# Kernel tuning notes

Measured on AMD Instinct MI355X. Metric: run time of the kernel, lower is better.

Reference implementation:

```python
import jax, jax.numpy as jnp
import numpy as np
from functools import partial

B, F, H, G, S = 8192, 16, 128, 4, 20  # batch, features, hidden, goals, SUBSTEPS
A_IZH, B_IZH, C_IZH, D_IZH = 0.02, 0.2, -65.0, 8.0  # Izhikevich 'RS' params
RATE_DECAY = 0.9
GAMMA, LR = 0.95, 1e-3


def izh_step(v, u, rate, I):
    """One Izhikevich substep (dt=1): returns new (v, u, rate, spike)."""
    v_new = v + (0.04 * v * v + 5.0 * v + 140.0 - u + I)
    u_new = u + A_IZH * (B_IZH * v - u)
    spike = (v_new >= 30.0).astype(v.dtype)
    v_new = jnp.where(spike > 0, C_IZH, v_new)
    u_new = u_new + spike * D_IZH
    rate_new = RATE_DECAY * rate + (1.0 - RATE_DECAY) * spike
    return v_new, u_new, rate_new, spike


def build_features(energy, threat, food_visible, goal, cls_probs, DA_, NA_):
    # [B,16] = [4 scalars | one-hot goal (4) | cls_probs (5) | DA | NA | hunger]
    base = jnp.stack([energy / 100.0, threat, food_visible, 1.0 - energy / 100.0], axis=-1)
    onehot = jax.nn.one_hot(goal, G, dtype=base.dtype)
    tail = jnp.stack([DA_, NA_, jnp.maximum(0.0, 0.5 - energy / 100.0)], axis=-1)
    return jnp.concatenate([base, onehot, cls_probs, tail], axis=-1)


def setup_inputs() -> dict:
    key = jax.random.key(0)
    ks = jax.random.split(key, 16)
    energy = jax.random.uniform(ks[0], (B,)) * 100.0
    threat = jax.random.uniform(ks[1], (B,))
    food_visible = jax.random.uniform(ks[2], (B,))
    goal = jax.random.randint(ks[3], (B,), 0, G)
    prev_goal = jax.random.randint(ks[4], (B,), 0, G)
    DA_ = jax.random.uniform(ks[5], (B,))
    NA_ = jax.random.uniform(ks[6], (B,))
    reward = jax.random.normal(ks[7], (B,)) * 0.5
    cls_probs = jax.nn.softmax(jax.random.normal(ks[8], (B, 5)), axis=-1)
    a_in = 0.5 * np.sqrt(6.0 / (F + H))   # xavier_uniform gain 0.5
    a_out = 0.3 * np.sqrt(6.0 / (H + G))  # xavier_uniform gain 0.3
    W_in_w = jax.random.uniform(ks[9], (B, H, F), minval=-a_in, maxval=a_in)
    W_in_b = jax.random.uniform(ks[10], (B, H), minval=-1.0, maxval=1.0) / np.sqrt(F)
    W_out_w = jax.random.uniform(ks[11], (B, G, H), minval=-a_out, maxval=a_out)
    W_out_b = jax.random.uniform(ks[12], (B, G), minval=-1.0, maxval=1.0) / np.sqrt(H)
    hv = jnp.full((B, H), -65.0)
    hu = B_IZH * hv
    hrate = jnp.zeros((B, H))
    vv = jnp.full((B, G), -65.0)
    vu = B_IZH * vv
    vrate = jnp.zeros((B, G))
    elig_in = jnp.zeros((B, H, F))
    elig_out = jnp.zeros((B, G, H))
    prev_values = jnp.zeros((B, G))
    prev_features = jax.random.uniform(ks[13], (B, F))
    noise = jax.random.normal(ks[14], (S, B, H))
    return dict(energy=energy, threat=threat, food_visible=food_visible, goal=goal,
                prev_goal=prev_goal, DA_=DA_, NA_=NA_, reward=reward, cls_probs=cls_probs,
                W_in_w=W_in_w, W_in_b=W_in_b, W_out_w=W_out_w, W_out_b=W_out_b,
                hv=hv, hu=hu, hrate=hrate, vv=vv, vu=vu, vrate=vrate,
                elig_in=elig_in, elig_out=elig_out, prev_values=prev_values,
                prev_features=prev_features, noise=noise)


def reference(energy, threat, food_visible, goal, prev_goal, DA_, NA_, reward, cls_probs,
              W_in_w, W_in_b, W_out_w, W_out_b, hv, hu, hrate, vv, vu, vrate,
              elig_in, elig_out, prev_values, prev_features, noise):
    features = build_features(energy, threat, food_visible, goal, cls_probs, DA_, NA_)  # [B,F]
    I_in = jnp.einsum('bhf,bf->bh', W_in_w, features) + W_in_b
    I_in = I_in * (5.0 / (jnp.mean(jnp.abs(I_in), axis=-1, keepdims=True) + 1e-8))

    def step(carry, nz):
        hv, hu, hrate, vv, vu, vrate, hsp, vsp = carry
        hv, hu, hrate, sp_h = izh_step(hv, hu, hrate, I_in + 0.3 * nz)
        I_out = jnp.einsum('bgh,bh->bg', W_out_w, hrate) + W_out_b
        I_out = I_out * (4.0 / (jnp.mean(jnp.abs(I_out), axis=-1, keepdims=True) + 1e-8))
        vv, vu, vrate, sp_v = izh_step(vv, vu, vrate, I_out)
        return (hv, hu, hrate, vv, vu, vrate, hsp + sp_h, vsp + sp_v), None

    carry0 = (hv, hu, hrate, vv, vu, vrate, jnp.zeros_like(hrate), jnp.zeros_like(vrate))
    (hv, hu, hrate, vv, vu, vrate, h_spikes, v_spikes), _ = jax.lax.scan(step, carry0, noise)

    values = jnp.einsum('bgh,bh->bg', W_out_w, hrate) + W_out_b  # [B,G]
    V_now = jnp.take_along_axis(values, goal[:, None], axis=1)[:, 0]
    V_prev = jnp.take_along_axis(prev_values, prev_goal[:, None], axis=1)[:, 0]
    td = reward + GAMMA * V_now - V_prev  # [B]

    elig_in_new = 0.9 * elig_in + hrate[:, :, None] * prev_features[:, None, :]
    elig_out_new = 0.9 * elig_out + vrate[:, :, None] * hrate[:, None, :]

    upd = (jnp.abs(td) > 1e-3)  # [B]
    scale = (LR * td * DA_)[:, None, None]
    W_in_new = jnp.where(upd[:, None, None], jnp.clip(W_in_w + scale * elig_in_new, -3.0, 3.0), W_in_w)
    W_out_new = jnp.where(upd[:, None, None], jnp.clip(W_out_w + scale * elig_out_new, -3.0, 3.0), W_out_w)

    hidden_active = jnp.mean((h_spikes > 0).astype(values.dtype), axis=-1)  # [B]
    return values, td, hidden_active, W_in_new, W_out_new, elig_in_new, elig_out_new
```

## Files before the change

kernel.cpp:

```cpp
#include <hip/hip_runtime.h>


namespace {

constexpr int F = 16;
constexpr int H = 128;
constexpr int G = 4;
constexpr int S = 20;

__device__ __forceinline__ float clip3(float x) {
    return fminf(fmaxf(x, -3.0f), 3.0f);
}

__global__ __launch_bounds__(128)
void spiking_critic_kernel(
    const float* __restrict__ energy,
    const float* __restrict__ threat,
    const float* __restrict__ food_visible,
    const int*   __restrict__ goal,
    const int*   __restrict__ prev_goal,
    const float* __restrict__ DA,
    const float* __restrict__ NA,
    const float* __restrict__ reward,
    const float* __restrict__ cls_probs,
    const float* __restrict__ W_in_w,
    const float* __restrict__ W_in_b,
    const float* __restrict__ W_out_w,
    const float* __restrict__ W_out_b,
    const float* __restrict__ hv_in,
    const float* __restrict__ hu_in,
    const float* __restrict__ hrate_in,
    const float* __restrict__ vv_in,
    const float* __restrict__ vu_in,
    const float* __restrict__ vrate_in,
    const float* __restrict__ elig_in,
    const float* __restrict__ elig_out,
    const float* __restrict__ prev_values,
    const float* __restrict__ prev_features,
    const float* __restrict__ noise,
    float* __restrict__ out_values,
    float* __restrict__ out_td,
    float* __restrict__ out_hidden,
    float* __restrict__ out_Win,
    float* __restrict__ out_Wout,
    float* __restrict__ out_ein,
    float* __restrict__ out_eout,
    int nB)
{
    const int b = blockIdx.x;
    const int t = threadIdx.x;

    __shared__ float w_in_lds[H * F];
    __shared__ float w_out_lds[G * H];
    __shared__ float feat[F];
    __shared__ float pf_lds[F];
    __shared__ float hrate_lds[H];
    __shared__ float wob[G];
    __shared__ float iout_lds[G];
    __shared__ float vals_lds[G];
    __shared__ float vrate_lds[G];
    __shared__ float red[2];
    __shared__ float tdsh;

    const float4* wi4 = (const float4*)(W_in_w + (size_t)b * (H * F));
    float4* wl4 = (float4*)w_in_lds;
    #pragma unroll
    for (int k = 0; k < 4; ++k) wl4[t + 128 * k] = wi4[t + 128 * k];
    ((float4*)w_out_lds)[t] = ((const float4*)(W_out_w + (size_t)b * (G * H)))[t];

    if (t < F) pf_lds[t] = prev_features[(size_t)b * F + t];
    if (t < G) wob[t]    = W_out_b[(size_t)b * G + t];

    if (t < F) {
        float e = energy[b];
        float v;
        if      (t == 0)  v = e / 100.0f;
        else if (t == 1)  v = threat[b];
        else if (t == 2)  v = food_visible[b];
        else if (t == 3)  v = 1.0f - e / 100.0f;
        else if (t < 8)   v = (goal[b] == (t - 4)) ? 1.0f : 0.0f;
        else if (t < 13)  v = cls_probs[(size_t)b * 5 + (t - 8)];
        else if (t == 13) v = DA[b];
        else if (t == 14) v = NA[b];
        else              v = fmaxf(0.0f, 0.5f - e / 100.0f);
        feat[t] = v;
    }
    __syncthreads();

    float dot = 0.0f;
    #pragma unroll
    for (int j = 0; j < 4; ++j) {
        float4 w = ((const float4*)w_in_lds)[t * 4 + j];
        dot += w.x * feat[4 * j + 0] + w.y * feat[4 * j + 1]
             + w.z * feat[4 * j + 2] + w.w * feat[4 * j + 3];
    }
    float Iraw = dot + W_in_b[(size_t)b * H + t];
    float a = fabsf(Iraw);
    #pragma unroll
    for (int m = 32; m >= 1; m >>= 1) a += __shfl_xor(a, m, 64);
    if ((t & 63) == 0) red[t >> 6] = a;
    __syncthreads();
    float meanI = (red[0] + red[1]) * (1.0f / 128.0f);
    float Iin = Iraw * (5.0f / (meanI + 1e-8f));

    float hv = hv_in[(size_t)b * H + t];
    float hu = hu_in[(size_t)b * H + t];
    float hr = hrate_in[(size_t)b * H + t];
    float hsp = 0.0f;
    float vvv = 0.0f, vuu = 0.0f, vrr = 0.0f;
    if (t < G) {
        vvv = vv_in[(size_t)b * G + t];
        vuu = vu_in[(size_t)b * G + t];
        vrr = vrate_in[(size_t)b * G + t];
    }

    float nz[S];
    #pragma unroll
    for (int s = 0; s < S; ++s)
        nz[s] = noise[((size_t)s * nB + b) * H + t];

    const int g = t >> 5;
    const int l = t & 31;

    #pragma unroll
    for (int s = 0; s < S; ++s) {
        float I  = Iin + 0.3f * nz[s];
        float vn = hv + (0.04f * hv * hv + 5.0f * hv + 140.0f - hu + I);
        float un = hu + 0.02f * (0.2f * hv - hu);
        float sp = (vn >= 30.0f) ? 1.0f : 0.0f;
        hv = (sp > 0.0f) ? -65.0f : vn;
        hu = un + sp * 8.0f;
        hr = 0.9f * hr + 0.1f * sp;
        hsp += sp;
        hrate_lds[t] = hr;
        __syncthreads();

        float p = 0.0f;
        #pragma unroll
        for (int k = 0; k < 4; ++k) {
            int h = l + 32 * k;
            p += w_out_lds[g * H + h] * hrate_lds[h];
        }
        #pragma unroll
        for (int m = 16; m >= 1; m >>= 1) p += __shfl_xor(p, m, 64);
        if (l == 0) iout_lds[g] = p + wob[g];
        __syncthreads();

        if (t < G) {
            float m4 = 0.25f * (fabsf(iout_lds[0]) + fabsf(iout_lds[1])
                              + fabsf(iout_lds[2]) + fabsf(iout_lds[3]));
            float Io  = iout_lds[t] * (4.0f / (m4 + 1e-8f));
            float vn2 = vvv + (0.04f * vvv * vvv + 5.0f * vvv + 140.0f - vuu + Io);
            float un2 = vuu + 0.02f * (0.2f * vvv - vuu);
            float spv = (vn2 >= 30.0f) ? 1.0f : 0.0f;
            vvv = (spv > 0.0f) ? -65.0f : vn2;
            vuu = un2 + spv * 8.0f;
            vrr = 0.9f * vrr + 0.1f * spv;
        }
    }

    if (t < G) vrate_lds[t] = vrr;
    float p = 0.0f;
    #pragma unroll
    for (int k = 0; k < 4; ++k) {
        int h = l + 32 * k;
        p += w_out_lds[g * H + h] * hrate_lds[h];
    }
    #pragma unroll
    for (int m = 16; m >= 1; m >>= 1) p += __shfl_xor(p, m, 64);
    if (l == 0) {
        float val = p + wob[g];
        vals_lds[g] = val;
        out_values[(size_t)b * G + g] = val;
    }

    unsigned long long mb = __ballot(hsp > 0.0f);
    if ((t & 63) == 0) red[t >> 6] = (float)__popcll(mb);
    __syncthreads();

    if (t == 0) {
        float Vnow  = vals_lds[goal[b]];
        float Vprev = prev_values[(size_t)b * G + prev_goal[b]];
        float td = reward[b] + 0.95f * Vnow - Vprev;
        out_td[b]     = td;
        out_hidden[b] = (red[0] + red[1]) * (1.0f / 128.0f);
        tdsh = td;
    }
    __syncthreads();

    const float td    = tdsh;
    const float scale = 1e-3f * td * DA[b];
    const bool  upd   = fabsf(td) > 1e-3f;

    {
        const float4* ei4 = (const float4*)(elig_in + (size_t)b * (H * F));
        float4* oW = (float4*)(out_Win + (size_t)b * (H * F));
        float4* oE = (float4*)(out_ein + (size_t)b * (H * F));
        const float4* pf4 = (const float4*)pf_lds;
        #pragma unroll
        for (int k = 0; k < 4; ++k) {
            int q = t + 128 * k;
            int h = q >> 2;
            int j = q & 3;
            float4 e  = ei4[q];
            float4 pf = pf4[j];
            float  hrv = hrate_lds[h];
            float4 en;
            en.x = 0.9f * e.x + hrv * pf.x;
            en.y = 0.9f * e.y + hrv * pf.y;
            en.z = 0.9f * e.z + hrv * pf.z;
            en.w = 0.9f * e.w + hrv * pf.w;
            oE[q] = en;
            float4 w = wl4[q];
            float4 wn;
            if (upd) {
                wn.x = clip3(w.x + scale * en.x);
                wn.y = clip3(w.y + scale * en.y);
                wn.z = clip3(w.z + scale * en.z);
                wn.w = clip3(w.w + scale * en.w);
            } else {
                wn = w;
            }
            oW[q] = wn;
        }
    }

    {
        const float4* eo4 = (const float4*)(elig_out + (size_t)b * (G * H));
        float4* oW = (float4*)(out_Wout + (size_t)b * (G * H));
        float4* oE = (float4*)(out_eout + (size_t)b * (G * H));
        int q  = t;
        int gg = q >> 5;
        int h0 = (q & 31) * 4;
        float4 e  = eo4[q];
        float  vrv = vrate_lds[gg];
        float4 en;
        en.x = 0.9f * e.x + vrv * hrate_lds[h0 + 0];
        en.y = 0.9f * e.y + vrv * hrate_lds[h0 + 1];
        en.z = 0.9f * e.z + vrv * hrate_lds[h0 + 2];
        en.w = 0.9f * e.w + vrv * hrate_lds[h0 + 3];
        oE[q] = en;
        float4 w = ((const float4*)w_out_lds)[q];
        float4 wn;
        if (upd) {
            wn.x = clip3(w.x + scale * en.x);
            wn.y = clip3(w.y + scale * en.y);
            wn.z = clip3(w.z + scale * en.z);
            wn.w = clip3(w.w + scale * en.w);
        } else {
            wn = w;
        }
        oW[q] = wn;
    }
}

}

extern "C" void kernel_launch(void* const* d_in, const int* in_sizes, int n_in,
                              void* d_out, int out_size, void* d_ws, size_t ws_size,
                              hipStream_t stream) {
    const int nB = in_sizes[0];

    float* out        = (float*)d_out;
    float* out_values = out;
    float* out_td     = out_values + (size_t)nB * G;
    float* out_hidden = out_td + nB;
    float* out_Win    = out_hidden + nB;
    float* out_Wout   = out_Win + (size_t)nB * H * F;
    float* out_ein    = out_Wout + (size_t)nB * G * H;
    float* out_eout   = out_ein + (size_t)nB * H * F;

    spiking_critic_kernel<<<dim3(nB), dim3(128), 0, stream>>>(
        (const float*)d_in[0],  (const float*)d_in[1],  (const float*)d_in[2],
        (const int*)  d_in[3],  (const int*)  d_in[4],
        (const float*)d_in[5],  (const float*)d_in[6],  (const float*)d_in[7],
        (const float*)d_in[8],  (const float*)d_in[9],  (const float*)d_in[10],
        (const float*)d_in[11], (const float*)d_in[12], (const float*)d_in[13],
        (const float*)d_in[14], (const float*)d_in[15], (const float*)d_in[16],
        (const float*)d_in[17], (const float*)d_in[18], (const float*)d_in[19],
        (const float*)d_in[20], (const float*)d_in[21], (const float*)d_in[22],
        (const float*)d_in[23],
        out_values, out_td, out_hidden, out_Win, out_Wout, out_ein, out_eout,
        nB);
}
```

Baseline: 394.8 us.

## Decouple hidden and value-layer recurrences to remove per-substep block barriers

The hidden-layer rate for every substep is now stored in shared memory (padded rows), so the 20-step hidden recurrence runs without barriers. The 80 output-current dot products are then computed in parallel by 80 threads, and the 4 value neurons run their recurrence serially afterwards. This removes the 40 __syncthreads per block that sat inside the substep loop. W_in is also read directly from global memory instead of being staged in LDS, which cuts LDS usage and may raise occupancy, at the cost of reading W_in from global twice. The serial value-layer tail on 4 threads and the strided per-row dot products add some latency.

```diff
diff --git a/kernel.cpp b/kernel.cpp
--- a/kernel.cpp
+++ b/kernel.cpp
@@ -7,6 +7,7 @@
 constexpr int H = 128;
 constexpr int G = 4;
 constexpr int S = 20;
+constexpr int HP = H + 1;
 
 __device__ __forceinline__ float clip3(float x) {
     return fminf(fmaxf(x, -3.0f), 3.0f);
@@ -50,24 +51,18 @@
     const int b = blockIdx.x;
     const int t = threadIdx.x;
 
-    __shared__ float w_in_lds[H * F];
     __shared__ float w_out_lds[G * H];
+    __shared__ float hrate_all[S * HP];
+    __shared__ float hrfin_lds[H];
     __shared__ float feat[F];
     __shared__ float pf_lds[F];
-    __shared__ float hrate_lds[H];
+    __shared__ float iout_all[S * G];
     __shared__ float wob[G];
-    __shared__ float iout_lds[G];
-    __shared__ float vals_lds[G];
     __shared__ float vrate_lds[G];
     __shared__ float red[2];
     __shared__ float tdsh;
 
-    const float4* wi4 = (const float4*)(W_in_w + (size_t)b * (H * F));
-    float4* wl4 = (float4*)w_in_lds;
-    #pragma unroll
-    for (int k = 0; k < 4; ++k) wl4[t + 128 * k] = wi4[t + 128 * k];
     ((float4*)w_out_lds)[t] = ((const float4*)(W_out_w + (size_t)b * (G * H)))[t];
-
     if (t < F) pf_lds[t] = prev_features[(size_t)b * F + t];
     if (t < G) wob[t]    = W_out_b[(size_t)b * G + t];
 
@@ -87,10 +82,11 @@
     }
     __syncthreads();
 
+    const float4* wrow = (const float4*)(W_in_w + ((size_t)b * H + t) * F);
     float dot = 0.0f;
     #pragma unroll
     for (int j = 0; j < 4; ++j) {
-        float4 w = ((const float4*)w_in_lds)[t * 4 + j];
+        float4 w = wrow[j];
         dot += w.x * feat[4 * j + 0] + w.y * feat[4 * j + 1]
              + w.z * feat[4 * j + 2] + w.w * feat[4 * j + 3];
     }
@@ -100,28 +96,19 @@
     for (int m = 32; m >= 1; m >>= 1) a += __shfl_xor(a, m, 64);
     if ((t & 63) == 0) red[t >> 6] = a;
     __syncthreads();
-    float meanI = (red[0] + red[1]) * (1.0f / 128.0f);
-    float Iin = Iraw * (5.0f / (meanI + 1e-8f));
+    const float meanI = (red[0] + red[1]) * (1.0f / 128.0f);
+    const float Iin = Iraw * (5.0f / (meanI + 1e-8f));
 
     float hv = hv_in[(size_t)b * H + t];
     float hu = hu_in[(size_t)b * H + t];
     float hr = hrate_in[(size_t)b * H + t];
-    float hsp = 0.0f;
-    float vvv = 0.0f, vuu = 0.0f, vrr = 0.0f;
-    if (t < G) {
-        vvv = vv_in[(size_t)b * G + t];
-        vuu = vu_in[(size_t)b * G + t];
-        vrr = vrate_in[(size_t)b * G + t];
-    }
 
     float nz[S];
     #pragma unroll
     for (int s = 0; s < S; ++s)
         nz[s] = noise[((size_t)s * nB + b) * H + t];
 
-    const int g = t >> 5;
-    const int l = t & 31;
-
+    float hsp = 0.0f;
     #pragma unroll
     for (int s = 0; s < S; ++s) {
         float I  = Iin + 0.3f * nz[s];
@@ -132,46 +119,47 @@
         hu = un + sp * 8.0f;
         hr = 0.9f * hr + 0.1f * sp;
         hsp += sp;
-        hrate_lds[t] = hr;
-        __syncthreads();
-
-        float p = 0.0f;
+        hrate_all[s * HP + t] = hr;
+    }
+    hrfin_lds[t] = hr;
+    __syncthreads();
+
+    if (t < S * G) {
+        const int s = t >> 2;
+        const int g = t & 3;
+        const float* __restrict__ wr   = w_out_lds + g * H;
+        const float* __restrict__ hrow = hrate_all + s * HP;
+        float acc = 0.0f;
+        #pragma unroll 8
+        for (int i = 0; i < H; ++i) {
+            int h = (i + t) & (H - 1);
+            acc = fmaf(wr[h], hrow[h], acc);
+        }
+        iout_all[t] = acc + wob[g];
+    }
+    __syncthreads();
+
+    if (t < G) {
+        float vvv = vv_in[(size_t)b * G + t];
+        float vuu = vu_in[(size_t)b * G + t];
+        float vrr = vrate_in[(size_t)b * G + t];
         #pragma unroll
-        for (int k = 0; k < 4; ++k) {
-            int h = l + 32 * k;
-            p += w_out_lds[g * H + h] * hrate_lds[h];
-        }
-        #pragma unroll
-        for (int m = 16; m >= 1; m >>= 1) p += __shfl_xor(p, m, 64);
-        if (l == 0) iout_lds[g] = p + wob[g];
-        __syncthreads();
-
-        if (t < G) {
-            float m4 = 0.25f * (fabsf(iout_lds[0]) + fabsf(iout_lds[1])
-                              + fabsf(iout_lds[2]) + fabsf(iout_lds[3]));
-            float Io  = iout_lds[t] * (4.0f / (m4 + 1e-8f));
-            float vn2 = vvv + (0.04f * vvv * vvv + 5.0f * vvv + 140.0f - vuu + Io);
-            float un2 = vuu + 0.02f * (0.2f * vvv - vuu);
-            float spv = (vn2 >= 30.0f) ? 1.0f : 0.0f;
-            vvv = (spv > 0.0f) ? -65.0f : vn2;
-            vuu = un2 + spv * 8.0f;
-            vrr = 0.9f * vrr + 0.1f * spv;
-        }
-    }
-
-    if (t < G) vrate_lds[t] = vrr;
-    float p = 0.0f;
-    #pragma unroll
-    for (int k = 0; k < 4; ++k) {
-        int h = l + 32 * k;
-        p += w_out_lds[g * H + h] * hrate_lds[h];
-    }
-    #pragma unroll
-    for (int m = 16; m >= 1; m >>= 1) p += __shfl_xor(p, m, 64);
-    if (l == 0) {
-        float val = p + wob[g];
-        vals_lds[g] = val;
-        out_values[(size_t)b * G + g] = val;
+        for (int s = 0; s < S; ++s) {
+            float i0 = iout_all[4 * s + 0];
+            float i1 = iout_all[4 * s + 1];
+            float i2 = iout_all[4 * s + 2];
+            float i3 = iout_all[4 * s + 3];
+            float m4 = 0.25f * (fabsf(i0) + fabsf(i1) + fabsf(i2) + fabsf(i3));
+            float Io = iout_all[4 * s + t] * (4.0f / (m4 + 1e-8f));
+            float vn = vvv + (0.04f * vvv * vvv + 5.0f * vvv + 140.0f - vuu + Io);
+            float un = vuu + 0.02f * (0.2f * vvv - vuu);
+            float sp = (vn >= 30.0f) ? 1.0f : 0.0f;
+            vvv = (sp > 0.0f) ? -65.0f : vn;
+            vuu = un + sp * 8.0f;
+            vrr = 0.9f * vrr + 0.1f * sp;
+        }
+        vrate_lds[t] = vrr;
+        out_values[(size_t)b * G + t] = iout_all[4 * (S - 1) + t];
     }
 
     unsigned long long mb = __ballot(hsp > 0.0f);
@@ -179,7 +167,7 @@
     __syncthreads();
 
     if (t == 0) {
-        float Vnow  = vals_lds[goal[b]];
+        float Vnow  = iout_all[4 * (S - 1) + goal[b]];
         float Vprev = prev_values[(size_t)b * G + prev_goal[b]];
         float td = reward[b] + 0.95f * Vnow - Vprev;
         out_td[b]     = td;
@@ -194,6 +182,7 @@
 
     {
         const float4* ei4 = (const float4*)(elig_in + (size_t)b * (H * F));
+        const float4* wi4 = (const float4*)(W_in_w  + (size_t)b * (H * F));
         float4* oW = (float4*)(out_Win + (size_t)b * (H * F));
         float4* oE = (float4*)(out_ein + (size_t)b * (H * F));
         const float4* pf4 = (const float4*)pf_lds;
@@ -204,14 +193,14 @@
             int j = q & 3;
             float4 e  = ei4[q];
             float4 pf = pf4[j];
-            float  hrv = hrate_lds[h];
+            float  hrv = hrfin_lds[h];
             float4 en;
             en.x = 0.9f * e.x + hrv * pf.x;
             en.y = 0.9f * e.y + hrv * pf.y;
             en.z = 0.9f * e.z + hrv * pf.z;
             en.w = 0.9f * e.w + hrv * pf.w;
             oE[q] = en;
-            float4 w = wl4[q];
+            float4 w = wi4[q];
             float4 wn;
             if (upd) {
                 wn.x = clip3(w.x + scale * en.x);
@@ -235,10 +224,10 @@
         float4 e  = eo4[q];
         float  vrv = vrate_lds[gg];
         float4 en;
-        en.x = 0.9f * e.x + vrv * hrate_lds[h0 + 0];
-        en.y = 0.9f * e.y + vrv * hrate_lds[h0 + 1];
-        en.z = 0.9f * e.z + vrv * hrate_lds[h0 + 2];
-        en.w = 0.9f * e.w + vrv * hrate_lds[h0 + 3];
+        en.x = 0.9f * e.x + vrv * hrfin_lds[h0 + 0];
+        en.y = 0.9f * e.y + vrv * hrfin_lds[h0 + 1];
+        en.z = 0.9f * e.z + vrv * hrfin_lds[h0 + 2];
+        en.w = 0.9f * e.w + vrv * hrfin_lds[h0 + 3];
         oE[q] = en;
         float4 w = ((const float4*)w_out_lds)[q];
         float4 wn;
```

Measured after the change: 393.7 us. Within noise of the previous version (-0.3%).
